# Optimization experiments

Hardware: AMD Instinct MI355X
Metric: run time of the kernel (lower is better)

Reference implementation:

```python
import jax, jax.numpy as jnp
import numpy as np

NUM_HEADS = 8


def setup_inputs() -> dict:
    key = jax.random.key(0)
    ks = jax.random.split(key, 6)
    B, C, H, W = 64, 512, 16, 16
    x = jax.random.normal(ks[0], (B, C, H, W), dtype=jnp.float32)
    qkv_w = jax.random.normal(ks[1], (3 * C, C), dtype=jnp.float32) * (C ** -0.5)
    qkv_b = jax.random.normal(ks[2], (3 * C,), dtype=jnp.float32) * 0.02
    out_w = jax.random.normal(ks[3], (C, C), dtype=jnp.float32) * (C ** -0.5)
    out_b = jax.random.normal(ks[4], (C,), dtype=jnp.float32) * 0.02
    rel_pos_enc = jax.random.normal(ks[5], (NUM_HEADS, 2 * 16 - 1, 2 * 16 - 1), dtype=jnp.float32) * 0.02
    return {"x": x, "qkv_w": qkv_w, "qkv_b": qkv_b, "out_w": out_w,
            "out_b": out_b, "rel_pos_enc": rel_pos_enc}


def _attention(x, qkv_w, qkv_b, out_w, out_b, rel_pos_enc):
    B, C, H, W = x.shape
    heads = rel_pos_enc.shape[0]
    hd = C // heads
    N = H * W

    # 1x1 conv qkv projection == pointwise GEMM over channels
    qkv = jnp.einsum('bchw,oc->bohw', x, qkv_w) + qkv_b[None, :, None, None]
    q, k, v = jnp.split(qkv, 3, axis=1)  # each (B, C, H, W)
    q = q.reshape(B, heads, hd, N)
    k = k.reshape(B, heads, hd, N)
    v = v.reshape(B, heads, hd, N)

    attn = jnp.einsum('bhdn,bhdm->bhnm', q, k) * (hd ** -0.5)  # (B,h,N,N)

    # gathered 2D relative position bias: bias[head,(h1,w1),(h2,w2)] =
    #   rel_pos_enc[head, h1-h2+15, w1-w2+15]
    h_idx = (jnp.arange(H)[:, None] - jnp.arange(H)[None, :]) + 16 - 1  # (H,H)
    w_idx = (jnp.arange(W)[:, None] - jnp.arange(W)[None, :]) + 16 - 1  # (W,W)
    bias = rel_pos_enc[:, h_idx[:, None, :, None], w_idx[None, :, None, :]]  # (h,H,W,H,W)
    bias = bias.reshape(heads, N, N)

    attn = jax.nn.softmax(attn + bias[None], axis=-1)
    out = jnp.einsum('bhnm,bhdm->bhdn', attn, v).reshape(B, C, H, W)
    out = jnp.einsum('bchw,oc->bohw', out, out_w) + out_b[None, :, None, None]
    return out


def reference(x, qkv_w, qkv_b, out_w, out_b, rel_pos_enc):
    return _attention(x, qkv_w, qkv_b, out_w, out_b, rel_pos_enc)
```

## Files before the change

kernel.cpp:

```cpp
#include <hip/hip_runtime.h>

typedef __attribute__((ext_vector_type(8))) short short8;
typedef __attribute__((ext_vector_type(4))) float floatx4;

#define MFMA16(a,b,c) __builtin_amdgcn_mfma_f32_16x16x32_bf16((a),(b),(c),0,0,0)

static __device__ __forceinline__ unsigned short f2bf(float f){
    unsigned int u = __float_as_uint(f);
    u = (u + 0x7FFFu + ((u >> 16) & 1u)) >> 16;
    return (unsigned short)u;
}

static __device__ __forceinline__ void async16(const unsigned short* g, unsigned short* l){
    __builtin_amdgcn_global_load_lds(
        (const __attribute__((address_space(1))) unsigned int*)g,
        (__attribute__((address_space(3))) unsigned int*)l, 16, 0, 0);
}

__global__ __launch_bounds__(256) void k_prep(const float* __restrict__ x,
                                              unsigned short* __restrict__ xT,
                                              const float* __restrict__ qkvw,
                                              unsigned short* __restrict__ wqkv,
                                              const float* __restrict__ outw,
                                              unsigned short* __restrict__ wout){
    __shared__ unsigned short tile[64][72];
    const int bid = blockIdx.x;
    const int tid = threadIdx.x;
    if (bid < 2048){
        const int c0 = (bid & 7) * 64;
        const int n0 = ((bid >> 3) & 3) * 64;
        const int b  = bid >> 5;
        const int chunk = tid & 7;
        const int r     = tid >> 3;
        const float*    src = x  + (size_t)b * 131072;
        unsigned short* dst = xT + (size_t)b * 131072;
#pragma unroll
        for (int it = 0; it < 2; ++it){
            int c = r + it * 32;
            const float* p = src + (size_t)(c0 + c) * 256 + n0 + chunk * 8;
            float4 f0 = *(const float4*)(p);
            float4 f1 = *(const float4*)(p + 4);
            short8 v;
            v[0]=(short)f2bf(f0.x); v[1]=(short)f2bf(f0.y); v[2]=(short)f2bf(f0.z); v[3]=(short)f2bf(f0.w);
            v[4]=(short)f2bf(f1.x); v[5]=(short)f2bf(f1.y); v[6]=(short)f2bf(f1.z); v[7]=(short)f2bf(f1.w);
            *(short8*)&tile[c][chunk * 8] = v;
        }
        __syncthreads();
#pragma unroll
        for (int it = 0; it < 2; ++it){
            int n = r + it * 32;
            short8 o;
#pragma unroll
            for (int e = 0; e < 8; ++e) o[e] = (short)tile[chunk * 8 + e][n];
            *(short8*)(dst + (size_t)(n0 + n) * 512 + c0 + chunk * 8) = o;
        }
    } else {
        int i = (bid - 2048) * 256 + tid;
        const float* s; unsigned short* d; int j;
        if (i < 196608){ s = qkvw; d = wqkv; j = i; }
        else { j = i - 196608; if (j >= 65536) return; s = outw; d = wout; }
        float4 f = *(const float4*)(s + (size_t)j * 4);
        uint2 v;
        v.x = (unsigned int)f2bf(f.x) | ((unsigned int)f2bf(f.y) << 16);
        v.y = (unsigned int)f2bf(f.z) | ((unsigned int)f2bf(f.w) << 16);
        *(uint2*)(d + (size_t)j * 4) = v;
    }
}

__global__ __launch_bounds__(256, 2) void k_qkv(const unsigned short* __restrict__ xT,
                                                const unsigned short* __restrict__ wbf,
                                                const float* __restrict__ bias,
                                                unsigned short* __restrict__ qk,
                                                unsigned short* __restrict__ vh){
    __shared__ unsigned short Ash[2][128][32];
    __shared__ unsigned short Bsh[2][128][32];
    const int bid  = blockIdx.x;
    const int xcd  = bid & 7;
    const int slot = bid >> 3;
    const int t0 = (xcd * 16 + (slot & 15)) * 128;
    const int o0 = (slot >> 4) * 128;
    const bool is_v = (o0 >= 1024);
    const int tid  = threadIdx.x;
    const int wave = tid >> 6;
    const int lane = tid & 63;
    const int lrow = lane & 15;
    const int lk8  = (lane >> 4) * 8;
    const int wm   = (wave >> 1) * 64;
    const int wn   = (wave & 1) * 64;
    const int ld_row = wave * 32 + (lane >> 2);
    const int ld_col = (lane & 3) * 8;

    floatx4 acc[4][4];
#pragma unroll
    for (int i = 0; i < 4; ++i)
#pragma unroll
        for (int j = 0; j < 4; ++j){ floatx4 z = {0.f,0.f,0.f,0.f}; acc[i][j] = z; }

    const unsigned short* gA = xT  + (size_t)(t0 + ld_row) * 512 + ld_col;
    const unsigned short* gB = wbf + (size_t)(o0 + ld_row) * 512 + ld_col;

    for (int kk = 0; kk < 512; kk += 64){
        async16(gA + kk,                 &Ash[0][wave * 32][0]);
        async16(gA + kk + 16 * 512,      &Ash[0][wave * 32 + 16][0]);
        async16(gA + kk + 32,            &Ash[1][wave * 32][0]);
        async16(gA + kk + 32 + 16 * 512, &Ash[1][wave * 32 + 16][0]);
        async16(gB + kk,                 &Bsh[0][wave * 32][0]);
        async16(gB + kk + 16 * 512,      &Bsh[0][wave * 32 + 16][0]);
        async16(gB + kk + 32,            &Bsh[1][wave * 32][0]);
        async16(gB + kk + 32 + 16 * 512, &Bsh[1][wave * 32 + 16][0]);
        __syncthreads();
#pragma unroll
        for (int s = 0; s < 2; ++s){
            short8 af[4], bf[4];
#pragma unroll
            for (int mt = 0; mt < 4; ++mt)
                af[mt] = *(const short8*)(is_v ? &Bsh[s][wm + mt*16 + lrow][lk8]
                                               : &Ash[s][wm + mt*16 + lrow][lk8]);
#pragma unroll
            for (int nt = 0; nt < 4; ++nt)
                bf[nt] = *(const short8*)(is_v ? &Ash[s][wn + nt*16 + lrow][lk8]
                                               : &Bsh[s][wn + nt*16 + lrow][lk8]);
#pragma unroll
            for (int mt = 0; mt < 4; ++mt)
#pragma unroll
                for (int nt = 0; nt < 4; ++nt)
                    acc[mt][nt] = MFMA16(af[mt], bf[nt], acc[mt][nt]);
        }
        __syncthreads();
    }

    if (!is_v){
#pragma unroll
        for (int mt = 0; mt < 4; ++mt){
            int trow = t0 + wm + mt*16 + (lane >> 4) * 4;
#pragma unroll
            for (int nt = 0; nt < 4; ++nt){
                int oc = o0 + wn + nt*16 + lrow;
                float bv = bias[oc];
#pragma unroll
                for (int r = 0; r < 4; ++r)
                    qk[(size_t)(trow + r) * 1024 + oc] = f2bf(acc[mt][nt][r] + bv);
            }
        }
    } else {
#pragma unroll
        for (int mt = 0; mt < 4; ++mt){
            int orow0 = o0 + wm + mt*16 + (lane >> 4) * 4;
#pragma unroll
            for (int nt = 0; nt < 4; ++nt){
                int tcol = t0 + wn + nt*16 + lrow;
                int bb = tcol >> 8, nn = tcol & 255;
#pragma unroll
                for (int r = 0; r < 4; ++r){
                    float bv = bias[orow0 + r];
                    vh[(size_t)(bb * 512 + (orow0 + r - 1024)) * 256 + nn] =
                        f2bf(acc[mt][nt][r] + bv);
                }
            }
        }
    }
}

__global__ __launch_bounds__(512) void k_attn(const unsigned short* __restrict__ qk,
                                              const unsigned short* __restrict__ vh,
                                              const float* __restrict__ rel,
                                              unsigned short* __restrict__ ao){
    __shared__ unsigned short Ksh[256][72];
    __shared__ unsigned short Vsh[64][264];
    __shared__ unsigned short Plds[8][16][264];
    __shared__ float Relsh[961];
    const int h = blockIdx.x;
    const int b = blockIdx.y;
    const int tid  = threadIdx.x;
    const int wave = tid >> 6;
    const int lane = tid & 63;
    const int lrow = lane & 15;
    const int lgrp = lane >> 4;
    const int lk8  = lgrp * 8;
    const unsigned short* qbase = qk + (size_t)(b * 256) * 1024 + h * 64;
    const unsigned short* kbase = qbase + 512;
    const unsigned short* vbase = vh + (size_t)(b * 512 + h * 64) * 256;
    unsigned short* aob = ao + (size_t)(b * 256) * 512 + h * 64;

#pragma unroll
    for (int it = 0; it < 4; ++it){
        int idx = tid + it * 512;
        int kr = idx >> 3, kc = (idx & 7) * 8;
        *(short8*)&Ksh[kr][kc] = *(const short8*)(kbase + (size_t)kr * 1024 + kc);
        int vr = idx >> 5, vc = (idx & 31) * 8;
        *(short8*)&Vsh[vr][vc] = *(const short8*)(vbase + (size_t)vr * 256 + vc);
    }
    for (int i = tid; i < 961; i += 512) Relsh[i] = rel[h * 961 + i];

    short8 aq[2][2];
#pragma unroll
    for (int pp = 0; pp < 2; ++pp){
        int nr = wave * 32 + pp * 16 + lrow;
        aq[pp][0] = *(const short8*)(qbase + (size_t)nr * 1024 + lk8);
        aq[pp][1] = *(const short8*)(qbase + (size_t)nr * 1024 + 32 + lk8);
    }
    __syncthreads();

#pragma unroll
    for (int pp = 0; pp < 2; ++pp){
        const int nrow0 = wave * 32 + pp * 16;
        floatx4 s[16];
#pragma unroll
        for (int ct = 0; ct < 16; ++ct){
            short8 b0 = *(const short8*)&Ksh[ct * 16 + lrow][lk8];
            short8 b1 = *(const short8*)&Ksh[ct * 16 + lrow][32 + lk8];
            floatx4 z = {0.f,0.f,0.f,0.f};
            z = MFMA16(aq[pp][0], b0, z);
            z = MFMA16(aq[pp][1], b1, z);
            s[ct] = z;
        }
        float inv[4];
#pragma unroll
        for (int r = 0; r < 4; ++r){
            int n  = nrow0 + lgrp * 4 + r;
            int nh = n >> 4, nw = n & 15;
            float sum = 0.f;
#pragma unroll
            for (int ct = 0; ct < 16; ++ct){
                float bv = Relsh[(nh - ct + 15) * 31 + (nw - lrow + 15)];
                float e = __expf(s[ct][r] * 0.125f + bv);
                s[ct][r] = e;
                sum += e;
            }
#pragma unroll
            for (int off = 1; off < 16; off <<= 1)
                sum += __shfl_xor(sum, off, 64);
            inv[r] = 1.f / sum;
        }
#pragma unroll
        for (int ct = 0; ct < 16; ++ct)
#pragma unroll
            for (int r = 0; r < 4; ++r)
                Plds[wave][lgrp * 4 + r][ct * 16 + lrow] = f2bf(s[ct][r]);
        short8 pa[8];
#pragma unroll
        for (int ms = 0; ms < 8; ++ms)
            pa[ms] = *(const short8*)&Plds[wave][lrow][ms * 32 + lk8];
#pragma unroll
        for (int dt = 0; dt < 4; ++dt){
            floatx4 accO = {0.f,0.f,0.f,0.f};
#pragma unroll
            for (int ms = 0; ms < 8; ++ms){
                short8 vb = *(const short8*)&Vsh[dt * 16 + lrow][ms * 32 + lk8];
                accO = MFMA16(pa[ms], vb, accO);
            }
#pragma unroll
            for (int r = 0; r < 4; ++r){
                int n = nrow0 + lgrp * 4 + r;
                aob[(size_t)n * 512 + dt * 16 + lrow] = f2bf(accO[r] * inv[r]);
            }
        }
    }
}

__global__ __launch_bounds__(256, 2) void k_out(const unsigned short* __restrict__ ao,
                                                const unsigned short* __restrict__ wbf,
                                                const float* __restrict__ bias,
                                                float* __restrict__ out){
    __shared__ unsigned short Ash[2][128][32];
    __shared__ unsigned short Bsh[2][128][32];
    const int bid  = blockIdx.x;
    const int xcd  = bid & 7;
    const int slot = bid >> 3;
    const int t0 = (xcd * 16 + (slot & 15)) * 128;
    const int o0 = (slot >> 4) * 128;
    const int tid  = threadIdx.x;
    const int wave = tid >> 6;
    const int lane = tid & 63;
    const int lrow = lane & 15;
    const int lk8  = (lane >> 4) * 8;
    const int wm   = (wave >> 1) * 64;
    const int wn   = (wave & 1) * 64;
    const int ld_row = wave * 32 + (lane >> 2);
    const int ld_col = (lane & 3) * 8;

    floatx4 acc[4][4];
#pragma unroll
    for (int i = 0; i < 4; ++i)
#pragma unroll
        for (int j = 0; j < 4; ++j){ floatx4 z = {0.f,0.f,0.f,0.f}; acc[i][j] = z; }

    const unsigned short* gA = wbf + (size_t)(o0 + ld_row) * 512 + ld_col;
    const unsigned short* gB = ao  + (size_t)(t0 + ld_row) * 512 + ld_col;

    for (int kk = 0; kk < 512; kk += 64){
        async16(gA + kk,                 &Ash[0][wave * 32][0]);
        async16(gA + kk + 16 * 512,      &Ash[0][wave * 32 + 16][0]);
        async16(gA + kk + 32,            &Ash[1][wave * 32][0]);
        async16(gA + kk + 32 + 16 * 512, &Ash[1][wave * 32 + 16][0]);
        async16(gB + kk,                 &Bsh[0][wave * 32][0]);
        async16(gB + kk + 16 * 512,      &Bsh[0][wave * 32 + 16][0]);
        async16(gB + kk + 32,            &Bsh[1][wave * 32][0]);
        async16(gB + kk + 32 + 16 * 512, &Bsh[1][wave * 32 + 16][0]);
        __syncthreads();
#pragma unroll
        for (int s = 0; s < 2; ++s){
            short8 af[4], bf[4];
#pragma unroll
            for (int mt = 0; mt < 4; ++mt) af[mt] = *(const short8*)&Ash[s][wm + mt*16 + lrow][lk8];
#pragma unroll
            for (int nt = 0; nt < 4; ++nt) bf[nt] = *(const short8*)&Bsh[s][wn + nt*16 + lrow][lk8];
#pragma unroll
            for (int mt = 0; mt < 4; ++mt)
#pragma unroll
                for (int nt = 0; nt < 4; ++nt)
                    acc[mt][nt] = MFMA16(af[mt], bf[nt], acc[mt][nt]);
        }
        __syncthreads();
    }
#pragma unroll
    for (int mt = 0; mt < 4; ++mt){
        int orow0 = o0 + wm + mt*16 + (lane >> 4) * 4;
#pragma unroll
        for (int nt = 0; nt < 4; ++nt){
            int tcol = t0 + wn + nt*16 + lrow;
            int bb = tcol >> 8, nn = tcol & 255;
#pragma unroll
            for (int r = 0; r < 4; ++r){
                float bv = bias[orow0 + r];
                out[(size_t)(bb * 512 + orow0 + r) * 256 + nn] = acc[mt][nt][r] + bv;
            }
        }
    }
}

extern "C" void kernel_launch(void* const* d_in, const int* in_sizes, int n_in,
                              void* d_out, int out_size, void* d_ws, size_t ws_size,
                              hipStream_t stream){
    const float* x    = (const float*)d_in[0];
    const float* qkvw = (const float*)d_in[1];
    const float* qkvb = (const float*)d_in[2];
    const float* outw = (const float*)d_in[3];
    const float* outb = (const float*)d_in[4];
    const float* rel  = (const float*)d_in[5];
    float* out = (float*)d_out;

    const size_t XT_OFF = 0;
    const size_t QK_OFF = XT_OFF + 16777216;
    const size_t VH_OFF = QK_OFF + 33554432;
    const size_t W_OFF  = VH_OFF + 16777216;
    const size_t NEED   = W_OFF + 16777216;
    if (ws_size < NEED) return;

    char* ws = (char*)d_ws;
    unsigned short* xT = (unsigned short*)(ws + XT_OFF);
    unsigned short* ao = (unsigned short*)(ws + XT_OFF);
    unsigned short* qk = (unsigned short*)(ws + QK_OFF);
    unsigned short* vh = (unsigned short*)(ws + VH_OFF);
    unsigned short* wqkv_bf = (unsigned short*)(ws + W_OFF);
    unsigned short* wout_bf = (unsigned short*)(ws + W_OFF + 2097152);

    hipLaunchKernelGGL(k_prep, dim3(3072), dim3(256), 0, stream,
                       x, xT, qkvw, wqkv_bf, outw, wout_bf);
    hipLaunchKernelGGL(k_qkv,  dim3(1536), dim3(256), 0, stream, xT, wqkv_bf, qkvb, qk, vh);
    hipLaunchKernelGGL(k_attn, dim3(8, 64), dim3(512), 0, stream, qk, vh, rel, ao);
    hipLaunchKernelGGL(k_out,  dim3(512),  dim3(256), 0, stream, ao, wout_bf, outb, out);
}
```

Baseline: 169.2 us.

## Fuse QKV projection into attention kernel per batch-head with swizzled LDS

Replaces the separate QKV GEMM and attention kernels with one kernel in which each block computes Q, K and V for one (batch, head) pair directly into LDS and then runs attention on them. This removes the global round trip of the q/k/v intermediates (tens of MB of bf16 writes and reads) and one launch. LDS layouts use XOR swizzling to avoid bank conflicts, and the P buffer reuses the Q region. The cost is a large LDS footprint (~156 KB), which limits occupancy, and only 512 blocks of 512 threads.

```diff
diff --git a/kernel.cpp b/kernel.cpp
--- a/kernel.cpp
+++ b/kernel.cpp
@@ -11,7 +11,7 @@
     return (unsigned short)u;
 }
 
-static __device__ __forceinline__ void async16(const unsigned short* g, unsigned short* l){
+static __device__ __forceinline__ void async16(const unsigned short* g, const unsigned short* l){
     __builtin_amdgcn_global_load_lds(
         (const __attribute__((address_space(1))) unsigned int*)g,
         (__attribute__((address_space(3))) unsigned int*)l, 16, 0, 0);
@@ -67,192 +67,199 @@
     }
 }
 
-__global__ __launch_bounds__(256, 2) void k_qkv(const unsigned short* __restrict__ xT,
-                                                const unsigned short* __restrict__ wbf,
-                                                const float* __restrict__ bias,
-                                                unsigned short* __restrict__ qk,
-                                                unsigned short* __restrict__ vh){
-    __shared__ unsigned short Ash[2][128][32];
-    __shared__ unsigned short Bsh[2][128][32];
+__global__ __launch_bounds__(512, 2) void k_fused(const unsigned short* __restrict__ xT,
+                                                  const unsigned short* __restrict__ wbf,
+                                                  const float* __restrict__ qkvb,
+                                                  const float* __restrict__ rel,
+                                                  unsigned short* __restrict__ ao){
+    __shared__ unsigned short SH[79748];
+    const int XS = 0;
+    const int WS = 16384;
+    const int QS = 28672;
+    const int KS = 45056;
+    const int VS = 61440;
+    float* Relsh = (float*)&SH[77824];
+
     const int bid  = blockIdx.x;
     const int xcd  = bid & 7;
     const int slot = bid >> 3;
-    const int t0 = (xcd * 16 + (slot & 15)) * 128;
-    const int o0 = (slot >> 4) * 128;
-    const bool is_v = (o0 >= 1024);
-    const int tid  = threadIdx.x;
-    const int wave = tid >> 6;
-    const int lane = tid & 63;
-    const int lrow = lane & 15;
-    const int lk8  = (lane >> 4) * 8;
-    const int wm   = (wave >> 1) * 64;
-    const int wn   = (wave & 1) * 64;
-    const int ld_row = wave * 32 + (lane >> 2);
-    const int ld_col = (lane & 3) * 8;
-
-    floatx4 acc[4][4];
-#pragma unroll
-    for (int i = 0; i < 4; ++i)
-#pragma unroll
-        for (int j = 0; j < 4; ++j){ floatx4 z = {0.f,0.f,0.f,0.f}; acc[i][j] = z; }
-
-    const unsigned short* gA = xT  + (size_t)(t0 + ld_row) * 512 + ld_col;
-    const unsigned short* gB = wbf + (size_t)(o0 + ld_row) * 512 + ld_col;
-
-    for (int kk = 0; kk < 512; kk += 64){
-        async16(gA + kk,                 &Ash[0][wave * 32][0]);
-        async16(gA + kk + 16 * 512,      &Ash[0][wave * 32 + 16][0]);
-        async16(gA + kk + 32,            &Ash[1][wave * 32][0]);
-        async16(gA + kk + 32 + 16 * 512, &Ash[1][wave * 32 + 16][0]);
-        async16(gB + kk,                 &Bsh[0][wave * 32][0]);
-        async16(gB + kk + 16 * 512,      &Bsh[0][wave * 32 + 16][0]);
-        async16(gB + kk + 32,            &Bsh[1][wave * 32][0]);
-        async16(gB + kk + 32 + 16 * 512, &Bsh[1][wave * 32 + 16][0]);
-        __syncthreads();
-#pragma unroll
-        for (int s = 0; s < 2; ++s){
-            short8 af[4], bf[4];
-#pragma unroll
-            for (int mt = 0; mt < 4; ++mt)
-                af[mt] = *(const short8*)(is_v ? &Bsh[s][wm + mt*16 + lrow][lk8]
-                                               : &Ash[s][wm + mt*16 + lrow][lk8]);
-#pragma unroll
-            for (int nt = 0; nt < 4; ++nt)
-                bf[nt] = *(const short8*)(is_v ? &Ash[s][wn + nt*16 + lrow][lk8]
-                                               : &Bsh[s][wn + nt*16 + lrow][lk8]);
-#pragma unroll
-            for (int mt = 0; mt < 4; ++mt)
-#pragma unroll
-                for (int nt = 0; nt < 4; ++nt)
-                    acc[mt][nt] = MFMA16(af[mt], bf[nt], acc[mt][nt]);
-        }
-        __syncthreads();
-    }
-
-    if (!is_v){
-#pragma unroll
-        for (int mt = 0; mt < 4; ++mt){
-            int trow = t0 + wm + mt*16 + (lane >> 4) * 4;
-#pragma unroll
-            for (int nt = 0; nt < 4; ++nt){
-                int oc = o0 + wn + nt*16 + lrow;
-                float bv = bias[oc];
-#pragma unroll
-                for (int r = 0; r < 4; ++r)
-                    qk[(size_t)(trow + r) * 1024 + oc] = f2bf(acc[mt][nt][r] + bv);
-            }
-        }
-    } else {
-#pragma unroll
-        for (int mt = 0; mt < 4; ++mt){
-            int orow0 = o0 + wm + mt*16 + (lane >> 4) * 4;
-#pragma unroll
-            for (int nt = 0; nt < 4; ++nt){
-                int tcol = t0 + wn + nt*16 + lrow;
-                int bb = tcol >> 8, nn = tcol & 255;
-#pragma unroll
-                for (int r = 0; r < 4; ++r){
-                    float bv = bias[orow0 + r];
-                    vh[(size_t)(bb * 512 + (orow0 + r - 1024)) * 256 + nn] =
-                        f2bf(acc[mt][nt][r] + bv);
-                }
-            }
-        }
-    }
-}
-
-__global__ __launch_bounds__(512) void k_attn(const unsigned short* __restrict__ qk,
-                                              const unsigned short* __restrict__ vh,
-                                              const float* __restrict__ rel,
-                                              unsigned short* __restrict__ ao){
-    __shared__ unsigned short Ksh[256][72];
-    __shared__ unsigned short Vsh[64][264];
-    __shared__ unsigned short Plds[8][16][264];
-    __shared__ float Relsh[961];
-    const int h = blockIdx.x;
-    const int b = blockIdx.y;
+    const int b = xcd * 8 + (slot & 7);
+    const int h = slot >> 3;
     const int tid  = threadIdx.x;
     const int wave = tid >> 6;
     const int lane = tid & 63;
     const int lrow = lane & 15;
     const int lgrp = lane >> 4;
-    const int lk8  = lgrp * 8;
-    const unsigned short* qbase = qk + (size_t)(b * 256) * 1024 + h * 64;
-    const unsigned short* kbase = qbase + 512;
-    const unsigned short* vbase = vh + (size_t)(b * 512 + h * 64) * 256;
-    unsigned short* aob = ao + (size_t)(b * 256) * 512 + h * 64;
-
-#pragma unroll
-    for (int it = 0; it < 4; ++it){
-        int idx = tid + it * 512;
-        int kr = idx >> 3, kc = (idx & 7) * 8;
-        *(short8*)&Ksh[kr][kc] = *(const short8*)(kbase + (size_t)kr * 1024 + kc);
-        int vr = idx >> 5, vc = (idx & 31) * 8;
-        *(short8*)&Vsh[vr][vc] = *(const short8*)(vbase + (size_t)vr * 256 + vc);
-    }
+    const int mq = wave >> 1;
+    const int nh = wave & 1;
+
     for (int i = tid; i < 961; i += 512) Relsh[i] = rel[h * 961 + i];
 
+    floatx4 acc[4][6];
+#pragma unroll
+    for (int i = 0; i < 4; ++i)
+#pragma unroll
+        for (int j = 0; j < 6; ++j){ floatx4 z = {0.f,0.f,0.f,0.f}; acc[i][j] = z; }
+
+    const unsigned short* xb = xT + (size_t)(b * 256) * 512;
+    const unsigned short* xsrc[4]; const unsigned short* xdst[4];
+#pragma unroll
+    for (int c = 0; c < 4; ++c){
+        int s   = (c * 8 + wave) * 64 + lane;
+        int row = s >> 3, pch = s & 7;
+        int sch = pch ^ (row & 7);
+        xsrc[c] = xb + (size_t)row * 512 + sch * 8;
+        xdst[c] = &SH[XS + (c * 8 + wave) * 512];
+    }
+    const unsigned short* wsrc[3]; const unsigned short* wdst[3];
+#pragma unroll
+    for (int c = 0; c < 3; ++c){
+        int s   = (c * 8 + wave) * 64 + lane;
+        int row = s >> 3, pch = s & 7;
+        int sch = pch ^ (row & 7);
+        int grow = (row >> 6) * 512 + h * 64 + (row & 63);
+        wsrc[c] = wbf + (size_t)grow * 512 + sch * 8;
+        wdst[c] = &SH[WS + (c * 8 + wave) * 512];
+    }
+
+    for (int kk = 0; kk < 512; kk += 64){
+#pragma unroll
+        for (int c = 0; c < 4; ++c) async16(xsrc[c] + kk, xdst[c]);
+#pragma unroll
+        for (int c = 0; c < 3; ++c) async16(wsrc[c] + kk, wdst[c]);
+        __syncthreads();
+#pragma unroll
+        for (int ks = 0; ks < 2; ++ks){
+            short8 af[4], bf[6];
+#pragma unroll
+            for (int mt = 0; mt < 4; ++mt){
+                int row = mq * 64 + mt * 16 + lrow;
+                int pch = (ks * 4 + lgrp) ^ (row & 7);
+                af[mt] = *(const short8*)&SH[XS + row * 64 + pch * 8];
+            }
+#pragma unroll
+            for (int nt = 0; nt < 6; ++nt){
+                int row = nh * 96 + nt * 16 + lrow;
+                int pch = (ks * 4 + lgrp) ^ (row & 7);
+                bf[nt] = *(const short8*)&SH[WS + row * 64 + pch * 8];
+            }
+#pragma unroll
+            for (int mt = 0; mt < 4; ++mt)
+#pragma unroll
+                for (int nt = 0; nt < 6; ++nt)
+                    acc[mt][nt] = MFMA16(af[mt], bf[nt], acc[mt][nt]);
+        }
+        __syncthreads();
+    }
+
+#pragma unroll
+    for (int mt = 0; mt < 4; ++mt){
+#pragma unroll
+        for (int nt = 0; nt < 6; ++nt){
+            int col = nh * 96 + nt * 16 + lrow;
+            int seg = col >> 6, off = col & 63;
+            float bv = qkvb[seg * 512 + h * 64 + off];
+#pragma unroll
+            for (int r = 0; r < 4; ++r){
+                int token = mq * 64 + mt * 16 + lgrp * 4 + r;
+                unsigned short v = f2bf(acc[mt][nt][r] + bv);
+                if (seg == 2){
+                    int lch = token >> 3;
+                    int pch = (lch & 24) | ((lch & 7) ^ (off & 7));
+                    SH[VS + off * 256 + pch * 8 + (token & 7)] = v;
+                } else {
+                    int base = seg ? KS : QS;
+                    int pch  = (off >> 3) ^ (token & 7);
+                    SH[base + token * 64 + pch * 8 + (off & 7)] = v;
+                }
+            }
+        }
+    }
+    __syncthreads();
+
     short8 aq[2][2];
 #pragma unroll
-    for (int pp = 0; pp < 2; ++pp){
-        int nr = wave * 32 + pp * 16 + lrow;
-        aq[pp][0] = *(const short8*)(qbase + (size_t)nr * 1024 + lk8);
-        aq[pp][1] = *(const short8*)(qbase + (size_t)nr * 1024 + 32 + lk8);
-    }
-    __syncthreads();
-
-#pragma unroll
-    for (int pp = 0; pp < 2; ++pp){
-        const int nrow0 = wave * 32 + pp * 16;
-        floatx4 s[16];
+    for (int pp = 0; pp < 2; ++pp)
+#pragma unroll
+        for (int kc = 0; kc < 2; ++kc){
+            int row = wave * 32 + pp * 16 + lrow;
+            int pch = (kc * 4 + lgrp) ^ (row & 7);
+            aq[pp][kc] = *(const short8*)&SH[QS + row * 64 + pch * 8];
+        }
+
+    floatx4 s2[2][16];
+#pragma unroll
+    for (int pp = 0; pp < 2; ++pp)
 #pragma unroll
         for (int ct = 0; ct < 16; ++ct){
-            short8 b0 = *(const short8*)&Ksh[ct * 16 + lrow][lk8];
-            short8 b1 = *(const short8*)&Ksh[ct * 16 + lrow][32 + lk8];
+            int row = ct * 16 + lrow;
+            int pch0 = lgrp ^ (row & 7);
+            short8 b0 = *(const short8*)&SH[KS + row * 64 + pch0 * 8];
+            short8 b1 = *(const short8*)&SH[KS + row * 64 + (pch0 ^ 4) * 8];
             floatx4 z = {0.f,0.f,0.f,0.f};
             z = MFMA16(aq[pp][0], b0, z);
             z = MFMA16(aq[pp][1], b1, z);
-            s[ct] = z;
-        }
-        float inv[4];
+            s2[pp][ct] = z;
+        }
+
+    float inv[2][4];
+#pragma unroll
+    for (int pp = 0; pp < 2; ++pp)
 #pragma unroll
         for (int r = 0; r < 4; ++r){
-            int n  = nrow0 + lgrp * 4 + r;
-            int nh = n >> 4, nw = n & 15;
+            int n   = wave * 32 + pp * 16 + lgrp * 4 + r;
+            int nh_ = n >> 4, nw = n & 15;
             float sum = 0.f;
 #pragma unroll
             for (int ct = 0; ct < 16; ++ct){
-                float bv = Relsh[(nh - ct + 15) * 31 + (nw - lrow + 15)];
-                float e = __expf(s[ct][r] * 0.125f + bv);
-                s[ct][r] = e;
+                float e = __expf(s2[pp][ct][r] * 0.125f +
+                                 Relsh[(nh_ - ct + 15) * 31 + (nw - lrow + 15)]);
+                s2[pp][ct][r] = e;
                 sum += e;
             }
 #pragma unroll
             for (int off = 1; off < 16; off <<= 1)
                 sum += __shfl_xor(sum, off, 64);
-            inv[r] = 1.f / sum;
-        }
+            inv[pp][r] = 1.f / sum;
+        }
+
+    __syncthreads();
+
+    const int PB = QS + wave * 4096;
+    unsigned short* aob = ao + (size_t)(b * 256) * 512 + h * 64;
+#pragma unroll
+    for (int pp = 0; pp < 2; ++pp){
 #pragma unroll
         for (int ct = 0; ct < 16; ++ct)
 #pragma unroll
-            for (int r = 0; r < 4; ++r)
-                Plds[wave][lgrp * 4 + r][ct * 16 + lrow] = f2bf(s[ct][r]);
+            for (int r = 0; r < 4; ++r){
+                int row = lgrp * 4 + r;
+                int lch = ct * 2 + (lrow >> 3);
+                int pch = (lch & 24) | ((lch & 7) ^ (row & 7));
+                SH[PB + row * 256 + pch * 8 + (lrow & 7)] = f2bf(s2[pp][ct][r]);
+            }
         short8 pa[8];
 #pragma unroll
-        for (int ms = 0; ms < 8; ++ms)
-            pa[ms] = *(const short8*)&Plds[wave][lrow][ms * 32 + lk8];
+        for (int ms = 0; ms < 8; ++ms){
+            int lch = ms * 4 + lgrp;
+            int pch = (lch & 24) | ((lch & 7) ^ (lrow & 7));
+            pa[ms] = *(const short8*)&SH[PB + lrow * 256 + pch * 8];
+        }
 #pragma unroll
         for (int dt = 0; dt < 4; ++dt){
             floatx4 accO = {0.f,0.f,0.f,0.f};
 #pragma unroll
             for (int ms = 0; ms < 8; ++ms){
-                short8 vb = *(const short8*)&Vsh[dt * 16 + lrow][ms * 32 + lk8];
+                int row = dt * 16 + lrow;
+                int lch = ms * 4 + lgrp;
+                int pch = (lch & 24) | ((lch & 7) ^ (row & 7));
+                short8 vb = *(const short8*)&SH[VS + row * 256 + pch * 8];
                 accO = MFMA16(pa[ms], vb, accO);
             }
 #pragma unroll
             for (int r = 0; r < 4; ++r){
-                int n = nrow0 + lgrp * 4 + r;
-                aob[(size_t)n * 512 + dt * 16 + lrow] = f2bf(accO[r] * inv[r]);
+                int n = wave * 32 + pp * 16 + lgrp * 4 + r;
+                aob[(size_t)n * 512 + dt * 16 + lrow] = f2bf(accO[r] * inv[pp][r]);
             }
         }
     }
@@ -341,23 +348,21 @@
     float* out = (float*)d_out;
 
     const size_t XT_OFF = 0;
-    const size_t QK_OFF = XT_OFF + 16777216;
-    const size_t VH_OFF = QK_OFF + 33554432;
-    const size_t W_OFF  = VH_OFF + 16777216;
-    const size_t NEED   = W_OFF + 16777216;
+    const size_t AO_OFF = 16777216;
+    const size_t W_OFF  = 33554432;
+    const size_t NEED   = W_OFF + 4194304;
     if (ws_size < NEED) return;
 
     char* ws = (char*)d_ws;
     unsigned short* xT = (unsigned short*)(ws + XT_OFF);
-    unsigned short* ao = (unsigned short*)(ws + XT_OFF);
-    unsigned short* qk = (unsigned short*)(ws + QK_OFF);
-    unsigned short* vh = (unsigned short*)(ws + VH_OFF);
+    unsigned short* ao = (unsigned short*)(ws + AO_OFF);
     unsigned short* wqkv_bf = (unsigned short*)(ws + W_OFF);
     unsigned short* wout_bf = (unsigned short*)(ws + W_OFF + 2097152);
 
-    hipLaunchKernelGGL(k_prep, dim3(3072), dim3(256), 0, stream,
+    hipLaunchKernelGGL(k_prep,  dim3(3072), dim3(256), 0, stream,
                        x, xT, qkvw, wqkv_bf, outw, wout_bf);
-    hipLaunchKernelGGL(k_qkv,  dim3(1536), dim3(256), 0, stream, xT, wqkv_bf, qkvb, qk, vh);
-    hipLaunchKernelGGL(k_attn, dim3(8, 64), dim3(512), 0, stream, qk, vh, rel, ao);
-    hipLaunchKernelGGL(k_out,  dim3(512),  dim3(256), 0, stream, ao, wout_bf, outb, out);
-}
+    hipLaunchKernelGGL(k_fused, dim3(512),  dim3(512), 0, stream,
+                       xT, wqkv_bf, qkvb, rel, ao);
+    hipLaunchKernelGGL(k_out,   dim3(512),  dim3(256), 0, stream,
+                       ao, wout_bf, outb, out);
+}
```

After: 162.4 us. 1.04x faster.
